# Kernel tuning notes

Measured on AMD Instinct MI355X. Metric: run time of the kernel, lower is better.

Reference implementation:

```python
import jax, jax.numpy as jnp
import numpy as np


def setup_inputs() -> dict:
    key = jax.random.key(0)
    B, T, D = 16, 2048, 256
    inputs = jax.random.normal(key, (B, T, D), dtype=jnp.float32)
    return {"inputs": inputs, "window_size": 7}


def reference(inputs, window_size):
    # Faithful to the keras layer: output[b, t] = concat(x[t], x[t-1], ..., x[t-W+1])
    # with zeros where t-k < 0. Built with one pad + W shifted views instead of
    # the original O(W^2) pad/concat loop.
    B, T, D = inputs.shape
    W = window_size
    padded = jnp.pad(inputs, ((0, 0), (W - 1, 0), (0, 0)))  # [B, T+W-1, D]
    # slice k gives x shifted right by k (i.e., x[t-k]) over the valid range
    pieces = [padded[:, W - 1 - k : W - 1 - k + T, :] for k in range(W)]
    return jnp.concatenate(pieces, axis=2)  # [B, T, W*D]
```

## Files before the change

kernel.cpp:

```cpp
#include <hip/hip_runtime.h>
#include <hip/hip_bf16.h>


constexpr int B = 16;
constexpr int T = 2048;
constexpr int D = 256;
constexpr int W = 7;
constexpr int D4 = D / 4;
constexpr int ROW4 = W * D4;

__global__ __launch_bounds__(256) void window_embed_kernel(
    const float4* __restrict__ in, float4* __restrict__ out, int total4) {
  int i = blockIdx.x * blockDim.x + threadIdx.x;
  if (i >= total4) return;

  int row = i / ROW4;
  int rem = i - row * ROW4;
  int w   = rem / D4;
  int dd  = rem - w * D4;
  int t   = row & (T - 1);

  float4 v = make_float4(0.f, 0.f, 0.f, 0.f);
  int src_t = t - w;
  if (src_t >= 0) {
    v = in[(row - w) * D4 + dd];
  }
  out[i] = v;
}

extern "C" void kernel_launch(void* const* d_in, const int* in_sizes, int n_in,
                              void* d_out, int out_size, void* d_ws, size_t ws_size,
                              hipStream_t stream) {
  const float4* in = (const float4*)d_in[0];
  float4* out = (float4*)d_out;
  int total4 = out_size / 4;
  int block = 256;
  int grid = (total4 + block - 1) / block;
  window_embed_kernel<<<grid, block, 0, stream>>>(in, out, total4);
}
```

Measured before the change: 270.5 us.

## Scatter each input vector to its window slots and zero edges separately

The gather-per-output kernel becomes a scatter kernel. Each thread reads one input float4 once and writes it to up to seven output positions. A second small kernel writes the zero padding for the first W-1 timesteps of each batch. This removes the integer divisions per output element and the redundant input loads, at the cost of a second launch and more scattered store addresses.

Result: faster. 262.4 us (-3.0%).

```diff
diff --git a/kernel.cpp b/kernel.cpp
--- a/kernel.cpp
+++ b/kernel.cpp
@@ -2,30 +2,40 @@
 #include <hip/hip_bf16.h>
 
 
-constexpr int B = 16;
-constexpr int T = 2048;
-constexpr int D = 256;
-constexpr int W = 7;
+constexpr int B  = 16;
+constexpr int T  = 2048;
+constexpr int D  = 256;
+constexpr int W  = 7;
 constexpr int D4 = D / 4;
 constexpr int ROW4 = W * D4;
 
-__global__ __launch_bounds__(256) void window_embed_kernel(
-    const float4* __restrict__ in, float4* __restrict__ out, int total4) {
-  int i = blockIdx.x * blockDim.x + threadIdx.x;
-  if (i >= total4) return;
-
-  int row = i / ROW4;
-  int rem = i - row * ROW4;
-  int w   = rem / D4;
-  int dd  = rem - w * D4;
+__global__ __launch_bounds__(256) void window_scatter_kernel(
+    const float4* __restrict__ in, float4* __restrict__ out) {
+  int i = blockIdx.x * 256 + threadIdx.x;
+  int row = i >> 6;
+  int dd  = i & 63;
   int t   = row & (T - 1);
 
-  float4 v = make_float4(0.f, 0.f, 0.f, 0.f);
-  int src_t = t - w;
-  if (src_t >= 0) {
-    v = in[(row - w) * D4 + dd];
+  float4 v = in[i];
+  int base = row * ROW4 + dd;
+#pragma unroll
+  for (int w = 0; w < W; ++w) {
+    if (t + w < T) {
+      out[base + w * (ROW4 + D4)] = v;
+    }
   }
-  out[i] = v;
+}
+
+__global__ __launch_bounds__(256) void window_zero_edges_kernel(float4* __restrict__ out) {
+  int j = blockIdx.x * 256 + threadIdx.x;
+  if (j >= B * 21 * 64) return;
+  int dd = j & 63;
+  int p  = (j >> 6) % 21;
+  int b  = j / (21 * 64);
+  const unsigned char wv[21] = {1,2,2,3,3,3,4,4,4,4,5,5,5,5,5,6,6,6,6,6,6};
+  const unsigned char tv[21] = {0,0,1,0,1,2,0,1,2,3,0,1,2,3,4,0,1,2,3,4,5};
+  int w = wv[p], t = tv[p];
+  out[((b * T + t) * W + w) * D4 + dd] = make_float4(0.f, 0.f, 0.f, 0.f);
 }
 
 extern "C" void kernel_launch(void* const* d_in, const int* in_sizes, int n_in,
@@ -33,8 +43,10 @@
                               hipStream_t stream) {
   const float4* in = (const float4*)d_in[0];
   float4* out = (float4*)d_out;
-  int total4 = out_size / 4;
-  int block = 256;
-  int grid = (total4 + block - 1) / block;
-  window_embed_kernel<<<grid, block, 0, stream>>>(in, out, total4);
+
+  int total_in4 = B * T * D4;
+  window_scatter_kernel<<<total_in4 / 256, 256, 0, stream>>>(in, out);
+
+  int nz = B * 21 * 64;
+  window_zero_edges_kernel<<<(nz + 255) / 256, 256, 0, stream>>>(out);
 }
```
